# Kernel optimization log

Hardware: AMD Instinct MI355X
Metric: run time of the kernel (lower is better)

Reference implementation:

```python
import jax, jax.numpy as jnp
import numpy as np

B, T = 512, 16384


def ema(x, alpha):
    """Row-wise EMA: y_0 = x_0, y_t = alpha*x_t + (1-alpha)*y_{t-1}. x: [B, T]."""
    one_minus = 1.0 - alpha

    def step(carry, xt):  # carry: [B], xt: [B]
        y = alpha * xt + one_minus * carry
        return y, y

    init = x[:, 0]
    _, ys = jax.lax.scan(step, init, x[:, 1:].T)  # ys: [T-1, B]
    return jnp.concatenate([x[:, :1], ys.T], axis=1)  # [B, T]


def setup_inputs() -> dict:
    key = jax.random.key(0)
    data = jax.random.normal(key, (B, T), dtype=jnp.float32)
    return {"data": data, "short_period": 12, "long_period": 26, "signal_period": 9}


def reference(data, short_period, long_period, signal_period):
    short_alpha = 2.0 / (short_period + 1)
    long_alpha = 2.0 / (long_period + 1)
    signal_alpha = 2.0 / (signal_period + 1)
    macd_line = ema(data, short_alpha) - ema(data, long_alpha)
    signal_line = ema(macd_line, signal_alpha)
    hist = macd_line - signal_line
    return (macd_line, signal_line, hist)
```

## Files before the change

### kernel.cpp

```cpp
#include <hip/hip_runtime.h>


constexpr int kB = 512;
constexpr int kT = 16384;
constexpr int kSeg = 1024;
constexpr int kWarm = 256;
constexpr int kE = 20;
constexpr int kSegsPerRow = kT / kSeg;
constexpr int kWavesPerBlock = 4;

__device__ __forceinline__ float wave_scan_carry(float agg, float M, int lane) {
  float m = M;
  float z = agg;
#pragma unroll
  for (int i = 0; i < 6; ++i) {
    const int d = 1 << i;
    float t = __shfl_up(z, d, 64);
    if (lane >= d) z = fmaf(m, t, z);
    m = m * m;
  }
  float ex = __shfl_up(z, 1, 64);
  return (lane == 0) ? 0.0f : ex;
}

__device__ __forceinline__ float pow20(float b) {
  float b2 = b * b, b4 = b2 * b2, b8 = b4 * b4, b16 = b8 * b8;
  return b16 * b4;
}

__global__ __launch_bounds__(kWavesPerBlock * 64, 4)
void macd_kernel(const float* __restrict__ x,
                 const int* __restrict__ p_short,
                 const int* __restrict__ p_long,
                 const int* __restrict__ p_sig,
                 float* __restrict__ out) {
  const int lane    = threadIdx.x & 63;
  const int wave_id = (blockIdx.x * blockDim.x + threadIdx.x) >> 6;
  const int row     = wave_id / kSegsPerRow;
  const int seg     = wave_id % kSegsPerRow;
  const int s0      = seg * kSeg;

  const float a_s = 2.0f / (float)(p_short[0] + 1), b_s = 1.0f - a_s;
  const float a_l = 2.0f / (float)(p_long[0]  + 1), b_l = 1.0f - a_l;
  const float a_g = 2.0f / (float)(p_sig[0]   + 1), b_g = 1.0f - a_g;

  const float* xr = x + row * kT;
  const int base = s0 - kWarm + lane * kE;

  float xv[kE];
  if (base >= 0) {
#pragma unroll
    for (int j = 0; j < kE / 4; ++j) {
      const float4 v = *(const float4*)(xr + base + 4 * j);
      xv[4 * j + 0] = v.x; xv[4 * j + 1] = v.y;
      xv[4 * j + 2] = v.z; xv[4 * j + 3] = v.w;
    }
  } else {
#pragma unroll
    for (int i = 0; i < kE; ++i) {
      const int p = base + i;
      xv[i] = xr[p < 0 ? 0 : p];
    }
  }

  float ts = a_s * xv[0], tl = a_l * xv[0];
#pragma unroll
  for (int i = 1; i < kE; ++i) {
    ts = fmaf(b_s, ts, a_s * xv[i]);
    tl = fmaf(b_l, tl, a_l * xv[i]);
  }
  float cs = wave_scan_carry(ts, pow20(b_s), lane);
  float cl = wave_scan_carry(tl, pow20(b_l), lane);

  float m[kE];
#pragma unroll
  for (int i = 0; i < kE; ++i) {
    cs = fmaf(b_s, cs, a_s * xv[i]);
    cl = fmaf(b_l, cl, a_l * xv[i]);
    m[i] = cs - cl;
  }

  float tg = a_g * m[0];
#pragma unroll
  for (int i = 1; i < kE; ++i) tg = fmaf(b_g, tg, a_g * m[i]);
  float cg = wave_scan_carry(tg, pow20(b_g), lane);

  float* om = out + row * kT;
  float* og = om + kB * kT;
  float* oh = og + kB * kT;

#pragma unroll
  for (int j = 0; j < kE / 4; ++j) {
    float4 mv, gv, hv;
    mv.x = m[4 * j + 0]; mv.y = m[4 * j + 1];
    mv.z = m[4 * j + 2]; mv.w = m[4 * j + 3];
    cg = fmaf(b_g, cg, a_g * mv.x); gv.x = cg;
    cg = fmaf(b_g, cg, a_g * mv.y); gv.y = cg;
    cg = fmaf(b_g, cg, a_g * mv.z); gv.z = cg;
    cg = fmaf(b_g, cg, a_g * mv.w); gv.w = cg;
    const int e = lane * kE + 4 * j;
    if (e >= kWarm) {
      const int pos = s0 - kWarm + e;
      hv.x = mv.x - gv.x; hv.y = mv.y - gv.y;
      hv.z = mv.z - gv.z; hv.w = mv.w - gv.w;
      *(float4*)(om + pos) = mv;
      *(float4*)(og + pos) = gv;
      *(float4*)(oh + pos) = hv;
    }
  }
}

extern "C" void kernel_launch(void* const* d_in, const int* in_sizes, int n_in,
                              void* d_out, int out_size, void* d_ws, size_t ws_size,
                              hipStream_t stream) {
  const float* x = (const float*)d_in[0];
  const int* ps  = (const int*)d_in[1];
  const int* pl  = (const int*)d_in[2];
  const int* pg  = (const int*)d_in[3];
  float* out     = (float*)d_out;

  const int total_waves = kB * kSegsPerRow;
  const int blocks = total_waves / kWavesPerBlock;
  macd_kernel<<<blocks, kWavesPerBlock * 64, 0, stream>>>(x, ps, pl, pg, out);
}
```

Baseline: 145.7 us.

## Interleave lanes across float4 chunks with per-chunk wave scans for coalesced access

Each wave now processes its segment as five 256-element chunks where lane i owns four consecutive elements, instead of each lane owning 20 contiguous elements. Loads and float4 stores become fully coalesced across the wave, and the EMA carries are resolved with per-chunk wave scans (truncated to 4–5 shuffle levels) plus closed-form carry injection. This trades strided memory access for more shuffle instructions and relies on truncated lookback within the warmup window.

```diff
diff --git a/kernel.cpp b/kernel.cpp
--- a/kernel.cpp
+++ b/kernel.cpp
@@ -4,109 +4,131 @@
 constexpr int kB = 512;
 constexpr int kT = 16384;
 constexpr int kSeg = 1024;
-constexpr int kWarm = 256;
-constexpr int kE = 20;
+constexpr int kChunk = 256;
+constexpr int kChunks = 5;
 constexpr int kSegsPerRow = kT / kSeg;
-constexpr int kWavesPerBlock = 4;
+constexpr int kWPB = 4;
 
-__device__ __forceinline__ float wave_scan_carry(float agg, float M, int lane) {
-  float m = M;
-  float z = agg;
+template <int STEPS>
+__device__ __forceinline__ void wave_scan(float agg, float m0, int lane,
+                                          float& ex, float& tot) {
+  float m = m0, z = agg;
 #pragma unroll
-  for (int i = 0; i < 6; ++i) {
+  for (int i = 0; i < STEPS; ++i) {
     const int d = 1 << i;
     float t = __shfl_up(z, d, 64);
     if (lane >= d) z = fmaf(m, t, z);
     m = m * m;
   }
-  float ex = __shfl_up(z, 1, 64);
-  return (lane == 0) ? 0.0f : ex;
+  ex = __shfl_up(z, 1, 64);
+  if (lane == 0) ex = 0.0f;
+  tot = __shfl(z, 63, 64);
 }
 
-__device__ __forceinline__ float pow20(float b) {
-  float b2 = b * b, b4 = b2 * b2, b8 = b4 * b4, b16 = b8 * b8;
-  return b16 * b4;
+__device__ __forceinline__ float pow4lane(float b4, int lane) {
+  float m = b4, pw = 1.0f;
+#pragma unroll
+  for (int i = 0; i < 6; ++i) {
+    if (lane & (1 << i)) pw *= m;
+    m = m * m;
+  }
+  return pw;
 }
 
-__global__ __launch_bounds__(kWavesPerBlock * 64, 4)
+__global__ __launch_bounds__(kWPB * 64, 4)
 void macd_kernel(const float* __restrict__ x,
                  const int* __restrict__ p_short,
                  const int* __restrict__ p_long,
                  const int* __restrict__ p_sig,
                  float* __restrict__ out) {
-  const int lane    = threadIdx.x & 63;
-  const int wave_id = (blockIdx.x * blockDim.x + threadIdx.x) >> 6;
-  const int row     = wave_id / kSegsPerRow;
-  const int seg     = wave_id % kSegsPerRow;
-  const int s0      = seg * kSeg;
+  const int lane = threadIdx.x & 63;
+  const int wid  = (blockIdx.x * blockDim.x + threadIdx.x) >> 6;
+  const int row  = wid >> 4;
+  const int seg  = wid & (kSegsPerRow - 1);
+  const int p0   = seg * kSeg - kChunk;
 
   const float a_s = 2.0f / (float)(p_short[0] + 1), b_s = 1.0f - a_s;
   const float a_l = 2.0f / (float)(p_long[0]  + 1), b_l = 1.0f - a_l;
   const float a_g = 2.0f / (float)(p_sig[0]   + 1), b_g = 1.0f - a_g;
+  const float b2_s = b_s * b_s, b4_s = b2_s * b2_s;
+  const float b2_l = b_l * b_l, b4_l = b2_l * b2_l;
+  const float b2_g = b_g * b_g, b4_g = b2_g * b2_g;
+  const float pw_s = pow4lane(b4_s, lane);
+  const float pw_l = pow4lane(b4_l, lane);
+  const float pw_g = pow4lane(b4_g, lane);
 
   const float* xr = x + row * kT;
-  const int base = s0 - kWarm + lane * kE;
 
-  float xv[kE];
-  if (base >= 0) {
+  float4 xq[kChunks];
+  if (p0 >= 0) {
 #pragma unroll
-    for (int j = 0; j < kE / 4; ++j) {
-      const float4 v = *(const float4*)(xr + base + 4 * j);
-      xv[4 * j + 0] = v.x; xv[4 * j + 1] = v.y;
-      xv[4 * j + 2] = v.z; xv[4 * j + 3] = v.w;
-    }
+    for (int k = 0; k < kChunks; ++k)
+      xq[k] = *(const float4*)(xr + p0 + k * kChunk + lane * 4);
   } else {
+    const float x0v = xr[0];
+    xq[0] = make_float4(x0v, x0v, x0v, x0v);
 #pragma unroll
-    for (int i = 0; i < kE; ++i) {
-      const int p = base + i;
-      xv[i] = xr[p < 0 ? 0 : p];
-    }
+    for (int k = 1; k < kChunks; ++k)
+      xq[k] = *(const float4*)(xr + p0 + k * kChunk + lane * 4);
+  }
+  const float xfirst = __shfl(xq[0].x, 0, 64);
+
+  float ls[kChunks][4], ll[kChunks][4];
+  float exs[kChunks], Ts[kChunks], exl[kChunks], Tl[kChunks];
+#pragma unroll
+  for (int k = 0; k < kChunks; ++k) {
+    ls[k][0] = a_s * xq[k].x;
+    ls[k][1] = fmaf(b_s, ls[k][0], a_s * xq[k].y);
+    ls[k][2] = fmaf(b_s, ls[k][1], a_s * xq[k].z);
+    ls[k][3] = fmaf(b_s, ls[k][2], a_s * xq[k].w);
+    ll[k][0] = a_l * xq[k].x;
+    ll[k][1] = fmaf(b_l, ll[k][0], a_l * xq[k].y);
+    ll[k][2] = fmaf(b_l, ll[k][1], a_l * xq[k].z);
+    ll[k][3] = fmaf(b_l, ll[k][2], a_l * xq[k].w);
+    wave_scan<4>(ls[k][3], b4_s, lane, exs[k], Ts[k]);
+    wave_scan<5>(ll[k][3], b4_l, lane, exl[k], Tl[k]);
   }
 
-  float ts = a_s * xv[0], tl = a_l * xv[0];
+  float m[kChunks][4];
+  float lg[kChunks][4];
+  float exg[kChunks], Tg[kChunks];
 #pragma unroll
-  for (int i = 1; i < kE; ++i) {
-    ts = fmaf(b_s, ts, a_s * xv[i]);
-    tl = fmaf(b_l, tl, a_l * xv[i]);
+  for (int k = 0; k < kChunks; ++k) {
+    const float Cs = (k == 0) ? xfirst : Ts[k - 1];
+    const float Cl = (k == 0) ? xfirst : Tl[k - 1];
+    const float cin_s = fmaf(pw_s, Cs, exs[k]);
+    const float cin_l = fmaf(pw_l, Cl, exl[k]);
+    m[k][0] = fmaf(b_s, cin_s, ls[k][0]) - fmaf(b_l, cin_l, ll[k][0]);
+    m[k][1] = fmaf(b2_s, cin_s, ls[k][1]) - fmaf(b2_l, cin_l, ll[k][1]);
+    m[k][2] = fmaf(b2_s * b_s, cin_s, ls[k][2]) - fmaf(b2_l * b_l, cin_l, ll[k][2]);
+    m[k][3] = fmaf(b4_s, cin_s, ls[k][3]) - fmaf(b4_l, cin_l, ll[k][3]);
+    lg[k][0] = a_g * m[k][0];
+    lg[k][1] = fmaf(b_g, lg[k][0], a_g * m[k][1]);
+    lg[k][2] = fmaf(b_g, lg[k][1], a_g * m[k][2]);
+    lg[k][3] = fmaf(b_g, lg[k][2], a_g * m[k][3]);
+    wave_scan<4>(lg[k][3], b4_g, lane, exg[k], Tg[k]);
   }
-  float cs = wave_scan_carry(ts, pow20(b_s), lane);
-  float cl = wave_scan_carry(tl, pow20(b_l), lane);
-
-  float m[kE];
-#pragma unroll
-  for (int i = 0; i < kE; ++i) {
-    cs = fmaf(b_s, cs, a_s * xv[i]);
-    cl = fmaf(b_l, cl, a_l * xv[i]);
-    m[i] = cs - cl;
-  }
-
-  float tg = a_g * m[0];
-#pragma unroll
-  for (int i = 1; i < kE; ++i) tg = fmaf(b_g, tg, a_g * m[i]);
-  float cg = wave_scan_carry(tg, pow20(b_g), lane);
 
   float* om = out + row * kT;
   float* og = om + kB * kT;
   float* oh = og + kB * kT;
 
 #pragma unroll
-  for (int j = 0; j < kE / 4; ++j) {
+  for (int k = 1; k < kChunks; ++k) {
+    const float Cg = Tg[k - 1];
+    const float cin_g = fmaf(pw_g, Cg, exg[k]);
     float4 mv, gv, hv;
-    mv.x = m[4 * j + 0]; mv.y = m[4 * j + 1];
-    mv.z = m[4 * j + 2]; mv.w = m[4 * j + 3];
-    cg = fmaf(b_g, cg, a_g * mv.x); gv.x = cg;
-    cg = fmaf(b_g, cg, a_g * mv.y); gv.y = cg;
-    cg = fmaf(b_g, cg, a_g * mv.z); gv.z = cg;
-    cg = fmaf(b_g, cg, a_g * mv.w); gv.w = cg;
-    const int e = lane * kE + 4 * j;
-    if (e >= kWarm) {
-      const int pos = s0 - kWarm + e;
-      hv.x = mv.x - gv.x; hv.y = mv.y - gv.y;
-      hv.z = mv.z - gv.z; hv.w = mv.w - gv.w;
-      *(float4*)(om + pos) = mv;
-      *(float4*)(og + pos) = gv;
-      *(float4*)(oh + pos) = hv;
-    }
+    mv.x = m[k][0]; mv.y = m[k][1]; mv.z = m[k][2]; mv.w = m[k][3];
+    gv.x = fmaf(b_g, cin_g, lg[k][0]);
+    gv.y = fmaf(b2_g, cin_g, lg[k][1]);
+    gv.z = fmaf(b2_g * b_g, cin_g, lg[k][2]);
+    gv.w = fmaf(b4_g, cin_g, lg[k][3]);
+    hv.x = mv.x - gv.x; hv.y = mv.y - gv.y;
+    hv.z = mv.z - gv.z; hv.w = mv.w - gv.w;
+    const int pos = p0 + k * kChunk + lane * 4;
+    *(float4*)(om + pos) = mv;
+    *(float4*)(og + pos) = gv;
+    *(float4*)(oh + pos) = hv;
   }
 }
 
@@ -120,6 +142,6 @@
   float* out     = (float*)d_out;
 
   const int total_waves = kB * kSegsPerRow;
-  const int blocks = total_waves / kWavesPerBlock;
-  macd_kernel<<<blocks, kWavesPerBlock * 64, 0, stream>>>(x, ps, pl, pg, out);
+  const int blocks = total_waves / kWPB;
+  macd_kernel<<<blocks, kWPB * 64, 0, stream>>>(x, ps, pl, pg, out);
 }
```

Measured after the change: 132.9 us. 8.8% less time.
